# Optimization experiments

Measured on AMD Instinct MI355X. Metric: run time of the kernel, lower is better.

The kernel has to match this reference:

```python
import jax, jax.numpy as jnp
import numpy as np

NOT_EPSILON = 1.0

def swishmax(x, axis):
    # x * exp(x - max) normalized by sum(|.|) + 1 over `axis`
    xexp = x * jnp.exp(x - jnp.max(x, axis=axis, keepdims=True))
    return xexp / (jnp.sum(jnp.abs(xexp), axis=axis, keepdims=True) + NOT_EPSILON)

def setup_inputs() -> dict:
    key = jax.random.key(0)
    ks = jax.random.split(key, 8)
    B, S, D = 2, 512, 256
    std = 0.02
    x = jax.random.normal(ks[0], (B, S, D), dtype=jnp.float32)
    w_pre = jax.random.normal(ks[1], (D, D), dtype=jnp.float32) * std
    w_q   = jax.random.normal(ks[2], (D, D), dtype=jnp.float32) * std
    w_k   = jax.random.normal(ks[3], (D, D), dtype=jnp.float32) * std
    w_va  = jax.random.normal(ks[4], (D, D), dtype=jnp.float32) * std
    w_al  = jax.random.normal(ks[5], (D, D), dtype=jnp.float32) * std
    w_vo  = jax.random.normal(ks[6], (D, D), dtype=jnp.float32) * std
    w_end = jax.random.normal(ks[7], (D, D), dtype=jnp.float32) * std
    return {"x": x, "w_pre": w_pre, "w_q": w_q, "w_k": w_k,
            "w_va": w_va, "w_al": w_al, "w_vo": w_vo, "w_end": w_end}

def reference(x, w_pre, w_q, w_k, w_va, w_al, w_vo, w_end):
    # pre: module_1d = Linear(D, D, bias=False)
    X = x @ w_pre.T                                    # [B,S,D]
    # FractalAttention depth=2 (base case): row_dims=(-3,)
    q = X + X @ w_q.T                                  # residual query proj
    k = X + X @ w_k.T                                  # residual key proj
    # batchify: key lhs -> [B,Sk,1,D], query rhs -> [B,1,Sq,D]
    raw = k[:, :, None, :] * q[:, None, :, :]          # [B,Sk,Sq,D]
    logits = raw + raw @ w_al.T                        # residual logit proj over D
    scale = swishmax(logits, axis=-3)                  # normalize over Sk
    v = X + X @ w_va.T
    vs = v[:, :, None, :] * scale                      # [B,Sk,Sq,D]
    vsum = jnp.sum(vs, axis=-3)                        # [B,Sq,D]
    vout = vsum + vsum @ w_vo.T
    X = X + vout                                       # transformer residual
    X = X @ w_end.T                                    # end: module_1d
    return X
```

## Files before the change

### kernel.cpp

```cpp
#include <hip/hip_runtime.h>
#include <hip/hip_bf16.h>


typedef __attribute__((ext_vector_type(8))) short short8;
typedef __attribute__((ext_vector_type(4))) float f32x4;
typedef __attribute__((ext_vector_type(8))) _Float16 half8;
typedef __attribute__((ext_vector_type(4))) _Float16 half4;

#define DD 256
#define SS 512
#define LOG2E 1.4426950408889634f
#define LN2   0.6931471805599453f

__device__ __forceinline__ unsigned short f2bf(float f) {
  unsigned int b = __float_as_uint(f);
  b += 0x7FFFu + ((b >> 16) & 1u);
  return (unsigned short)(b >> 16);
}
__device__ __forceinline__ short8 cvt8(f32x4 lo, f32x4 hi) {
  short8 r;
  r[0]=(short)f2bf(lo[0]); r[1]=(short)f2bf(lo[1]);
  r[2]=(short)f2bf(lo[2]); r[3]=(short)f2bf(lo[3]);
  r[4]=(short)f2bf(hi[0]); r[5]=(short)f2bf(hi[1]);
  r[6]=(short)f2bf(hi[2]); r[7]=(short)f2bf(hi[3]);
  return r;
}

__global__ __launch_bounds__(256) void prep_weights(
    const float* __restrict__ w0, const float* __restrict__ w1,
    const float* __restrict__ w2, const float* __restrict__ w3,
    const float* __restrict__ w4, const float* __restrict__ w5,
    const float* __restrict__ wal, unsigned short* __restrict__ out)
{
  const int bi = blockIdx.x;
  const int m = bi >> 5;
  const int off = ((bi & 31) * 256 + threadIdx.x) * 8;
  const float* src = m==0?w0: m==1?w1: m==2?w2: m==3?w3: m==4?w4: m==5?w5: wal;
  f32x4 a = *(const f32x4*)(src + off);
  f32x4 b = *(const f32x4*)(src + off + 4);
  if (m == 6) {
    const int e = off >> 8, d = off & 255;
#pragma unroll
    for (int jj = 0; jj < 4; ++jj) {
      if (e == d + jj)     a[jj] += 1.0f;
      if (e == d + 4 + jj) b[jj] += 1.0f;
    }
    half8 h;
#pragma unroll
    for (int jj = 0; jj < 4; ++jj) {
      h[jj]     = (_Float16)a[jj];
      h[jj + 4] = (_Float16)b[jj];
    }
    *(half8*)(out + (size_t)m * 65536 + off) = h;
  } else {
    *(short8*)(out + (size_t)m * 65536 + off) = cvt8(a, b);
  }
}

__global__ __launch_bounds__(256) void linear_bf(
    const float* __restrict__ A, const unsigned short* __restrict__ Wbf,
    const float* __restrict__ res1, const float* __restrict__ res2,
    float* __restrict__ out)
{
  const int bi = blockIdx.x;
  const int rb = (bi >> 2) * 16;
  const int cb = (bi & 3) * 64;
  const int tid = threadIdx.x;
  const int wv = tid >> 6, lane = tid & 63;
  const int g = lane >> 4, c = lane & 15;
  const int arow = rb + c;
  const int wrow = cb + wv * 16 + c;

  f32x4 acc = (f32x4){0.f, 0.f, 0.f, 0.f};
#pragma unroll
  for (int ks = 0; ks < 8; ++ks) {
    const int d0 = ks * 32 + g * 8;
    f32x4 a0 = *(const f32x4*)(A + arow * DD + d0);
    f32x4 a1 = *(const f32x4*)(A + arow * DD + d0 + 4);
    short8 av = cvt8(a0, a1);
    short8 bv = *(const short8*)(Wbf + wrow * DD + d0);
    acc = __builtin_amdgcn_mfma_f32_16x16x32_bf16(av, bv, acc, 0, 0, 0);
  }
#pragma unroll
  for (int j = 0; j < 4; ++j) {
    const int ro = rb + g * 4 + j;
    const int co = cb + wv * 16 + c;
    float v = acc[j];
    if (res1) v += res1[ro * DD + co];
    if (res2) v += res2[ro * DD + co];
    out[ro * DD + co] = v;
  }
}

__global__ __launch_bounds__(256) void linear_qkv(
    const float* __restrict__ X,
    const unsigned short* __restrict__ Wq, const unsigned short* __restrict__ Wk,
    const unsigned short* __restrict__ Wv,
    _Float16* __restrict__ qout, _Float16* __restrict__ kout,
    _Float16* __restrict__ vout)
{
  const int bi = blockIdx.x;
  const int rb = (bi >> 2) * 16;
  const int cb = (bi & 3) * 64;
  const int tid = threadIdx.x;
  const int wv = tid >> 6, lane = tid & 63;
  const int g = lane >> 4, c = lane & 15;
  const int arow = rb + c;
  const int wrow = cb + wv * 16 + c;

  f32x4 aq = (f32x4){0.f,0.f,0.f,0.f};
  f32x4 ak = (f32x4){0.f,0.f,0.f,0.f};
  f32x4 av_ = (f32x4){0.f,0.f,0.f,0.f};
#pragma unroll
  for (int ks = 0; ks < 8; ++ks) {
    const int d0 = ks * 32 + g * 8;
    f32x4 a0 = *(const f32x4*)(X + arow * DD + d0);
    f32x4 a1 = *(const f32x4*)(X + arow * DD + d0 + 4);
    short8 af = cvt8(a0, a1);
    short8 bq = *(const short8*)(Wq + wrow * DD + d0);
    aq = __builtin_amdgcn_mfma_f32_16x16x32_bf16(af, bq, aq, 0, 0, 0);
    short8 bk = *(const short8*)(Wk + wrow * DD + d0);
    ak = __builtin_amdgcn_mfma_f32_16x16x32_bf16(af, bk, ak, 0, 0, 0);
    short8 bv = *(const short8*)(Wv + wrow * DD + d0);
    av_ = __builtin_amdgcn_mfma_f32_16x16x32_bf16(af, bv, av_, 0, 0, 0);
  }
#pragma unroll
  for (int j = 0; j < 4; ++j) {
    const int ro = rb + g * 4 + j;
    const int co = cb + wv * 16 + c;
    const float base = X[ro * DD + co];
    qout[ro * DD + co] = (_Float16)((base + aq[j]) * LOG2E);
    kout[ro * DD + co] = (_Float16)(base + ak[j]);
    vout[ro * DD + co] = (_Float16)(base + av_[j]);
  }
}

__global__ __launch_bounds__(256) void pack_kv(
    const _Float16* __restrict__ k, const _Float16* __restrict__ v,
    _Float16* __restrict__ kfrag, _Float16* __restrict__ vfrag)
{
  const int id = blockIdx.x * 256 + threadIdx.x;
  if (id < 32768) {
    const int lane = id & 63, ks = (id >> 6) & 7, t2 = (id >> 9) & 31, b = id >> 14;
    const int g = lane >> 4, c = lane & 15;
    const _Float16* src = k + ((size_t)(b * SS + t2 * 16 + c) * DD + ks * 32 + g * 8);
    *(half8*)(kfrag + (size_t)id * 8) = *(const half8*)src;
  } else {
    const int id2 = id - 32768;
    const int lane = id2 & 63, i = (id2 >> 6) & 1, slice = (id2 >> 7) & 7,
              t2 = (id2 >> 10) & 31, b = id2 >> 15;
    const int g = lane >> 4, c = lane & 15;
    const _Float16* src = v + ((size_t)(b * SS + t2 * 16 + c) * DD + slice * 32 + i * 16 + g * 4);
    *(half4*)(vfrag + (size_t)id2 * 4) = *(const half4*)src;
  }
}

__global__ __launch_bounds__(256, 3) void fractal_attn(
    const _Float16* __restrict__ walI,
    const _Float16* __restrict__ qf,
    const _Float16* __restrict__ kfrag,
    const _Float16* __restrict__ vfrag,
    float* __restrict__ vsum)
{
  const int bid = blockIdx.x;
  const int eh = bid & 1;
  const int sq = (bid >> 1) & 511;
  const int b  = bid >> 10;
  const int tid = threadIdx.x;
  const int wv = tid >> 6;
  const int lane = tid & 63;
  const int g = lane >> 4, c = lane & 15;
  const int slice = eh * 4 + wv;
  const int sbase = slice * 32;

  half8 afrag[2][8];
  {
    const _Float16* qrow = qf + (size_t)(b * SS + sq) * DD;
    half8 q8[8];
#pragma unroll
    for (int ks = 0; ks < 8; ++ks)
      q8[ks] = *(const half8*)(qrow + ks * 32 + g * 8);
#pragma unroll
    for (int i = 0; i < 2; ++i) {
      const int e = sbase + i * 16 + c;
      const _Float16* wrow = walI + (size_t)e * DD;
#pragma unroll
      for (int ks = 0; ks < 8; ++ks)
        afrag[i][ks] = (*(const half8*)(wrow + ks * 32 + g * 8)) * q8[ks];
    }
  }

  const _Float16* kfb = kfrag + (size_t)b * 131072 + lane * 8;
  const _Float16* vfb = vfrag + ((size_t)(b * 256 + slice) * 2) * 256 + lane * 4;

  float mst[8], sst[8], vst[8];
#pragma unroll
  for (int s = 0; s < 8; ++s) { mst[s] = -1e30f; sst[s] = 0.f; vst[s] = 0.f; }

  half8 bf[8];
  half4 vq[2];
  f32x4 acc[2];
  const f32x4 zeroc = (f32x4){0.f, 0.f, 0.f, 0.f};

#pragma unroll
  for (int ks = 0; ks < 8; ++ks) bf[ks] = *(const half8*)(kfb + ks * 512);
  vq[0] = *(const half4*)(vfb);
  vq[1] = *(const half4*)(vfb + 256);

#pragma unroll 1
  for (int t2 = 0; t2 < 32; ++t2) {
    __builtin_amdgcn_s_setprio(1);
    acc[0] = __builtin_amdgcn_mfma_f32_16x16x32_f16(afrag[0][0], bf[0], zeroc, 0, 0, 0);
    acc[1] = __builtin_amdgcn_mfma_f32_16x16x32_f16(afrag[1][0], bf[0], zeroc, 0, 0, 0);
#pragma unroll
    for (int ks = 1; ks < 8; ++ks) {
      acc[0] = __builtin_amdgcn_mfma_f32_16x16x32_f16(afrag[0][ks], bf[ks], acc[0], 0, 0, 0);
      acc[1] = __builtin_amdgcn_mfma_f32_16x16x32_f16(afrag[1][ks], bf[ks], acc[1], 0, 0, 0);
    }
    __builtin_amdgcn_s_setprio(0);

    if (t2 < 31) {
      const _Float16* kf_ = kfb + (t2 + 1) * 4096;
#pragma unroll
      for (int ks = 0; ks < 8; ++ks) bf[ks] = *(const half8*)(kf_ + ks * 512);
    }

#pragma unroll
    for (int i = 0; i < 2; ++i) {
#pragma unroll
      for (int j = 0; j < 4; ++j) {
        const int s = i * 4 + j;
        const float L = acc[i][j];
        mst[s] = fmaxf(mst[s], L);
        const float p = L * __builtin_amdgcn_exp2f(L);
        sst[s] += fabsf(p);
        vst[s] = fmaf((float)vq[i][j], p, vst[s]);
      }
    }

    if (t2 < 31) {
      const _Float16* vf_ = vfb + (t2 + 1) * 4096;
      vq[0] = *(const half4*)(vf_);
      vq[1] = *(const half4*)(vf_ + 256);
    }
  }

#pragma unroll
  for (int mask = 1; mask <= 8; mask <<= 1) {
#pragma unroll
    for (int s = 0; s < 8; ++s) {
      mst[s] = fmaxf(mst[s], __shfl_xor(mst[s], mask));
      sst[s] += __shfl_xor(sst[s], mask);
      vst[s] += __shfl_xor(vst[s], mask);
    }
  }

  if (c == 0) {
    float* orow = vsum + (size_t)(b * SS + sq) * DD;
#pragma unroll
    for (int i = 0; i < 2; ++i) {
      f32x4 o;
#pragma unroll
      for (int j = 0; j < 4; ++j) {
        const int s = i * 4 + j;
        const float tt = LN2 * __builtin_amdgcn_exp2f(-mst[s]);
        o[j] = vst[s] * tt / (sst[s] * tt + 1.0f);
      }
      *(f32x4*)(orow + sbase + i * 16 + g * 4) = o;
    }
  }
}

extern "C" void kernel_launch(void* const* d_in, const int* in_sizes, int n_in,
                              void* d_out, int out_size, void* d_ws, size_t ws_size,
                              hipStream_t stream) {
  const float* x     = (const float*)d_in[0];
  const float* w_pre = (const float*)d_in[1];
  const float* w_q   = (const float*)d_in[2];
  const float* w_k   = (const float*)d_in[3];
  const float* w_va  = (const float*)d_in[4];
  const float* w_al  = (const float*)d_in[5];
  const float* w_vo  = (const float*)d_in[6];
  const float* w_end = (const float*)d_in[7];
  float* out = (float*)d_out;

  char* ws = (char*)d_ws;
  float*    X     = (float*)(ws);
  float*    Y     = (float*)(ws + (1 << 20));
  float*    vsum  = (float*)(ws + (2 << 20));
  _Float16* qf16  = (_Float16*)(ws + (3 << 20));
  _Float16* kf16  = (_Float16*)(ws + (3 << 20) + (512 << 10));
  _Float16* vf16  = (_Float16*)(ws + (4 << 20));
  _Float16* kfrag = (_Float16*)(ws + (4 << 20) + (512 << 10));
  _Float16* vfrag = (_Float16*)(ws + (5 << 20));
  unsigned short* wbf = (unsigned short*)(ws + (5 << 20) + (512 << 10));

  prep_weights<<<224, 256, 0, stream>>>(w_pre, w_q, w_k, w_va, w_vo, w_end,
                                        w_al, wbf);
  linear_bf<<<256, 256, 0, stream>>>(x, wbf + 0 * 65536, nullptr, nullptr, X);
  linear_qkv<<<256, 256, 0, stream>>>(X, wbf + 1 * 65536, wbf + 2 * 65536,
                                      wbf + 3 * 65536, qf16, kf16, vf16);
  pack_kv<<<384, 256, 0, stream>>>(kf16, vf16, kfrag, vfrag);
  fractal_attn<<<2048, 256, 0, stream>>>((const _Float16*)(wbf + 6 * 65536),
                                         qf16, kfrag, vfrag, vsum);
  linear_bf<<<256, 256, 0, stream>>>(vsum, wbf + 4 * 65536, vsum, X, Y);
  linear_bf<<<256, 256, 0, stream>>>(Y, wbf + 5 * 65536, nullptr, nullptr, out);
}
```

Before: 137.2 us.

## Stage K/V fragments through LDS with async 4-deep global_load_lds pipeline

Replaces per-wave direct global register loads of K and V fragments in the attention loop with a block-cooperative 4-slot LDS ring filled by global_load_lds, prefetching three tiles ahead. Waves then read their fragments from LDS after an explicit vmcnt wait and a barrier. The intent is to share K tile loads across the four waves instead of each wave fetching the same data, and to hide global latency behind MFMA work. This adds 48KB of LDS per block, which may cut occupancy below the launch bound of 3, and adds a barrier on every iteration.

```diff
diff --git a/kernel.cpp b/kernel.cpp
--- a/kernel.cpp
+++ b/kernel.cpp
@@ -24,6 +24,12 @@
   r[4]=(short)f2bf(hi[0]); r[5]=(short)f2bf(hi[1]);
   r[6]=(short)f2bf(hi[2]); r[7]=(short)f2bf(hi[3]);
   return r;
+}
+__device__ __forceinline__ void gload16(const void* g, void* l) {
+  __builtin_amdgcn_global_load_lds(
+      (const __attribute__((address_space(1))) void*)g,
+      (__attribute__((address_space(3))) void*)l,
+      16, 0, 0);
 }
 
 __global__ __launch_bounds__(256) void prep_weights(
@@ -162,6 +168,9 @@
     const _Float16* __restrict__ vfrag,
     float* __restrict__ vsum)
 {
+  __shared__ _Float16 kt[4][4096];
+  __shared__ _Float16 vt[4][2048];
+
   const int bid = blockIdx.x;
   const int eh = bid & 1;
   const int sq = (bid >> 1) & 511;
@@ -173,6 +182,20 @@
   const int slice = eh * 4 + wv;
   const int sbase = slice * 32;
 
+  const _Float16* ktile0 = kfrag + (size_t)b * 131072;
+  const _Float16* vtile0 = vfrag + (size_t)b * 131072 + eh * 2048;
+  auto stage = [&](int t) {
+    const _Float16* ks = ktile0 + (size_t)t * 4096;
+    const _Float16* vs = vtile0 + (size_t)t * 4096;
+    _Float16* kd = &kt[t & 3][0];
+    _Float16* vd = &vt[t & 3][0];
+    gload16(ks + tid * 8,        kd + tid * 8);
+    gload16(ks + 2048 + tid * 8, kd + 2048 + tid * 8);
+    gload16(vs + tid * 8,        vd + tid * 8);
+  };
+
+  stage(0); stage(1); stage(2);
+
   half8 afrag[2][8];
   {
     const _Float16* qrow = qf + (size_t)(b * SS + sq) * DD;
@@ -190,9 +213,6 @@
     }
   }
 
-  const _Float16* kfb = kfrag + (size_t)b * 131072 + lane * 8;
-  const _Float16* vfb = vfrag + ((size_t)(b * 256 + slice) * 2) * 256 + lane * 4;
-
   float mst[8], sst[8], vst[8];
 #pragma unroll
   for (int s = 0; s < 8; ++s) { mst[s] = -1e30f; sst[s] = 0.f; vst[s] = 0.f; }
@@ -202,13 +222,23 @@
   f32x4 acc[2];
   const f32x4 zeroc = (f32x4){0.f, 0.f, 0.f, 0.f};
 
-#pragma unroll
-  for (int ks = 0; ks < 8; ++ks) bf[ks] = *(const half8*)(kfb + ks * 512);
-  vq[0] = *(const half4*)(vfb);
-  vq[1] = *(const half4*)(vfb + 256);
-
 #pragma unroll 1
-  for (int t2 = 0; t2 < 32; ++t2) {
+  for (int t = 0; t < 32; ++t) {
+    if (t < 30)      asm volatile("s_waitcnt vmcnt(6)" ::: "memory");
+    else if (t == 30) asm volatile("s_waitcnt vmcnt(3)" ::: "memory");
+    else              asm volatile("s_waitcnt vmcnt(0)" ::: "memory");
+    __builtin_amdgcn_s_barrier();
+
+    if (t + 3 < 32) stage(t + 3);
+
+    const _Float16* kb = &kt[t & 3][0];
+    const _Float16* vb = &vt[t & 3][0];
+#pragma unroll
+    for (int ks = 0; ks < 8; ++ks)
+      bf[ks] = *(const half8*)(kb + ks * 512 + lane * 8);
+    vq[0] = *(const half4*)(vb + wv * 512 + lane * 4);
+    vq[1] = *(const half4*)(vb + wv * 512 + 256 + lane * 4);
+
     __builtin_amdgcn_s_setprio(1);
     acc[0] = __builtin_amdgcn_mfma_f32_16x16x32_f16(afrag[0][0], bf[0], zeroc, 0, 0, 0);
     acc[1] = __builtin_amdgcn_mfma_f32_16x16x32_f16(afrag[1][0], bf[0], zeroc, 0, 0, 0);
@@ -218,12 +248,6 @@
       acc[1] = __builtin_amdgcn_mfma_f32_16x16x32_f16(afrag[1][ks], bf[ks], acc[1], 0, 0, 0);
     }
     __builtin_amdgcn_s_setprio(0);
-
-    if (t2 < 31) {
-      const _Float16* kf_ = kfb + (t2 + 1) * 4096;
-#pragma unroll
-      for (int ks = 0; ks < 8; ++ks) bf[ks] = *(const half8*)(kf_ + ks * 512);
-    }
 
 #pragma unroll
     for (int i = 0; i < 2; ++i) {
@@ -236,12 +260,6 @@
         sst[s] += fabsf(p);
         vst[s] = fmaf((float)vq[i][j], p, vst[s]);
       }
-    }
-
-    if (t2 < 31) {
-      const _Float16* vf_ = vfb + (t2 + 1) * 4096;
-      vq[0] = *(const half4*)(vf_);
-      vq[1] = *(const half4*)(vf_ + 256);
     }
   }
 
```

Result: faster. 131.9 us (-3.8%).
